# Performance work log

Measured on AMD Instinct MI355X. Metric: run time of the kernel, lower is better.

The kernel has to match this reference:

```python
import jax, jax.numpy as jnp
import numpy as np

B, S, T, E, H = 64, 256, 128, 256, 512


def setup_inputs() -> dict:
    key = jax.random.key(0)
    ks = jax.random.split(key, 12)
    sc = 0.05
    return {
        "trg_embed": jax.random.normal(ks[0], (B, T + 1, E), jnp.float32),
        "encoder_hidden": jax.random.normal(ks[1], (B, S, 2 * H), jnp.float32),
        "encoder_final": jax.random.normal(ks[2], (B, H), jnp.float32),
        "src_mask": jnp.ones((B, S), bool),
        "W_ih": jax.random.normal(ks[3], (3 * H, E + 2 * H), jnp.float32) * sc,
        "W_hh": jax.random.normal(ks[4], (3 * H, H), jnp.float32) * sc,
        "b_ih": jnp.zeros((3 * H,), jnp.float32),
        "b_hh": jnp.zeros((3 * H,), jnp.float32),
        "bridge_w": jax.random.normal(ks[5], (H, H), jnp.float32) * sc,
        "bridge_b": jnp.zeros((H,), jnp.float32),
        "key_w": jax.random.normal(ks[6], (H, 2 * H), jnp.float32) * sc,
        "query_w": jax.random.normal(ks[7], (H, H), jnp.float32) * sc,
        "energy_w": jax.random.normal(ks[8], (H,), jnp.float32) * sc,
        "pre_w": jax.random.normal(ks[9], (2 * H, H + 2 * H + E), jnp.float32) * sc,
        "pre_b": jnp.zeros((2 * H,), jnp.float32),
        "max_len": T,
    }


def reference(trg_embed, encoder_hidden, encoder_final, src_mask,
              W_ih, W_hh, b_ih, b_hh, bridge_w, bridge_b,
              key_w, query_w, energy_w, pre_w, pre_b, max_len):
    # bridge: initial decoder state from final encoder state
    h0 = jnp.tanh(encoder_final @ bridge_w.T + bridge_b)          # [B,H]
    # precomputed attention keys
    proj_key = jnp.einsum('bsk,hk->bsh', encoder_hidden, key_w)   # [B,S,H]
    neg = jnp.asarray(-1e9, trg_embed.dtype)

    prev = jnp.swapaxes(trg_embed[:, :max_len], 0, 1)             # [T,B,E]
    curr = jnp.swapaxes(trg_embed[:, 1:max_len + 1], 0, 1)        # [T,B,E] (generate_first)

    def step(h, pc):
        p, c = pc
        # --- additive (Bahdanau) attention, query = current hidden ---
        q = h @ query_w.T                                         # [B,H]
        scores = jnp.tanh(q[:, None, :] + proj_key) @ energy_w    # [B,S]
        scores = jnp.where(src_mask, scores, neg)
        alphas = jax.nn.softmax(scores, axis=-1)                  # [B,S]
        context = jnp.einsum('bs,bsd->bd', alphas, encoder_hidden)  # [B,2H]
        # --- generate_first: pre_output from previous hidden ---
        pre_out = jnp.concatenate([p, h, context], axis=-1) @ pre_w.T + pre_b  # [B,2H]
        # --- GRU cell (torch gate order r, z, n) ---
        x = jnp.concatenate([c, context], axis=-1)                # [B,E+2H]
        gi = x @ W_ih.T + b_ih
        gh = h @ W_hh.T + b_hh
        ir, iz, inn = jnp.split(gi, 3, axis=-1)
        hr, hz, hn = jnp.split(gh, 3, axis=-1)
        r = jax.nn.sigmoid(ir + hr)
        z = jax.nn.sigmoid(iz + hz)
        n = jnp.tanh(inn + r * hn)
        h_new = (1 - z) * n + z * h
        return h_new, (h_new, pre_out, alphas)

    h_fin, (states, pre_outs, attns) = jax.lax.scan(step, h0, (prev, curr))
    return (jnp.swapaxes(states, 0, 1),      # [B,T,H] decoder_states
            h_fin,                            # [B,H] final hidden
            jnp.swapaxes(pre_outs, 0, 1),     # [B,T,2H] pre_output_vectors
            jnp.swapaxes(attns, 0, 1))        # [B,T,S] attention_vectors
```

## Files before the change

kernel.cpp:

```cpp
#include <hip/hip_runtime.h>
#include <hip/hip_fp16.h>

using u32 = unsigned int;

constexpr int B = 64, S = 256, T = 128, E = 256, H = 512, H2 = 1024;
constexpr int TE = (T + 1) * E;

constexpr size_t OUT_HFIN = (size_t)B * T * H;
constexpr size_t OUT_PRE  = OUT_HFIN + (size_t)B * H;
constexpr size_t OUT_ATT  = OUT_PRE + (size_t)B * T * H2;

constexpr size_t WS_HPREV = 0;
constexpr size_t WS_QWT4  = 32768;
constexpr size_t WS_TRGT  = WS_QWT4 + 131072;
constexpr size_t WS_PK2   = WS_TRGT + 1056768;
constexpr size_t WS_HT2R  = WS_PK2 + 4194304;
constexpr size_t WS_QBUF  = WS_HT2R + 129 * 16384;
constexpr size_t WS_CTXR  = WS_QBUF + (size_t)128 * 16384;
constexpr size_t WS_SEWR  = WS_CTXR + (size_t)128 * 32768;
constexpr size_t WS_BAR   = WS_SEWR + 32768;
constexpr size_t WS_TOTAL = WS_BAR + 1024;

constexpr int L_EHS  = 0;
constexpr int L_EW   = 131072;
constexpr int L_HP   = 133376;
constexpr int L_SH2  = 134400;
constexpr int L_QRED = 135424;
constexpr int L_SHQ  = 135424;
constexpr int L_SCP  = 137728;
constexpr int L_SE   = 142080;
constexpr int L_CPAR = 142336;
constexpr int L_CRE1 = 135424;
constexpr int L_CRC  = 139520;
constexpr int L_SST  = 151808;
constexpr int SMEM_BYTES = 155904;

typedef _Float16 half8 __attribute__((ext_vector_type(8)));
typedef float    f32x4 __attribute__((ext_vector_type(4)));
union UH  { u32 u; _Float16 h[2]; };
union UH8 { uint4 v; half8 h; };

__device__ __forceinline__ u32 pkh(float a, float b) {
  auto v = __builtin_amdgcn_cvt_pkrtz(a, b);
  u32 r; __builtin_memcpy(&r, &v, 4); return r;
}
__device__ __forceinline__ float f16lo(u32 u) { UH x; x.u = u; return (float)x.h[0]; }
__device__ __forceinline__ float f16hi(u32 u) { UH x; x.u = u; return (float)x.h[1]; }

#if __has_builtin(__builtin_amdgcn_fdot2)
__device__ __forceinline__ float fdot2(u32 a, u32 b, float c) {
  typedef _Float16 h2t __attribute__((ext_vector_type(2)));
  h2t av, bv; __builtin_memcpy(&av, &a, 4); __builtin_memcpy(&bv, &b, 4);
  return __builtin_amdgcn_fdot2(av, bv, c, false);
}
#else
__device__ __forceinline__ float fdot2(u32 a, u32 b, float c) {
  return c + f16lo(a) * f16lo(b) + f16hi(a) * f16hi(b);
}
#endif

__device__ __forceinline__ float fast_tanh(float x) {
  return 1.0f - 2.0f / (__expf(2.0f * x) + 1.0f);
}
__device__ __forceinline__ float fast_sigmoid(float x) {
  return 1.0f / (1.0f + __expf(-x));
}
__device__ __forceinline__ float dot4(float4 a, float4 b) {
  return a.x * b.x + a.y * b.y + a.z * b.z + a.w * b.w;
}

__device__ __forceinline__ void st_wt(u32* p, u32 v) {
  __hip_atomic_store(p, v, __ATOMIC_RELAXED, __HIP_MEMORY_SCOPE_AGENT);
}
__device__ __forceinline__ void st_wt_f(float* p, float v) {
  union { float f; u32 u; } c; c.f = v;
  __hip_atomic_store((u32*)p, c.u, __ATOMIC_RELAXED, __HIP_MEMORY_SCOPE_AGENT);
}

__device__ __forceinline__ void gbar(u32* bar, int p, u32 n) {
  asm volatile("s_waitcnt vmcnt(0) lgkmcnt(0)" ::: "memory");
  __syncthreads();
  if (threadIdx.x == 0) {
    u32 old = __hip_atomic_fetch_add(bar + (p >> 4) * 32, 1u,
                                     __ATOMIC_RELAXED, __HIP_MEMORY_SCOPE_AGENT);
    if ((old & 15u) == 15u) {
      u32 r = __hip_atomic_fetch_add(bar + 768, 1u,
                                     __ATOMIC_RELAXED, __HIP_MEMORY_SCOPE_AGENT);
      if ((r & 15u) == 15u)
        __hip_atomic_store(bar + 800, n, __ATOMIC_RELAXED, __HIP_MEMORY_SCOPE_AGENT);
    }
    while (__hip_atomic_load(bar + 800, __ATOMIC_RELAXED,
                             __HIP_MEMORY_SCOPE_AGENT) < n)
      __builtin_amdgcn_s_sleep(2);
  }
  __syncthreads();
  asm volatile("" ::: "memory");
}

__global__ void bridge_kernel(const float* __restrict__ ef,
                              const float* __restrict__ bw,
                              const float* __restrict__ bb,
                              float* __restrict__ h0T) {
  int gid = blockIdx.x * blockDim.x + threadIdx.x;
  int j = gid >> 6, b = gid & 63;
  const float4* w = (const float4*)(bw + (size_t)j * H);
  const float4* e = (const float4*)(ef + (size_t)b * H);
  float acc = 0.f;
#pragma unroll 4
  for (int k = 0; k < H / 4; ++k) acc += dot4(w[k], e[k]);
  h0T[gid] = tanhf(acc + bb[j]);
}

__global__ void packh0_kernel(const float* __restrict__ hprevT, u32* __restrict__ hT2) {
  int idx = blockIdx.x * 512 + threadIdx.x;
  int dp = idx >> 6, b = idx & 63;
  hT2[(size_t)(dp >> 2) * 256 + b * 4 + (dp & 3)] =
      pkh(hprevT[(size_t)(2 * dp) * 64 + b], hprevT[(size_t)(2 * dp + 1) * 64 + b]);
}

__global__ void qwt4_kernel(const float* __restrict__ qw, uint4* __restrict__ qwt4) {
  int kq = blockIdx.x, j = threadIdx.x;
  const float* src = qw + (size_t)j * H + kq * 8;
  uint4 o;
  o.x = pkh(src[0], src[1]); o.y = pkh(src[2], src[3]);
  o.z = pkh(src[4], src[5]); o.w = pkh(src[6], src[7]);
  qwt4[(size_t)kq * 512 + j] = o;
}

__global__ void trgT2_kernel(const float* __restrict__ trg, u32* __restrict__ trgT) {
  int b = blockIdx.x, tid = threadIdx.x;
  for (int i = 0; i < 33; ++i) {
    int idx = i * 512 + tid;
    if (idx >= 129 * 128) break;
    int tt = idx >> 7, kp = idx & 127;
    float2 v = *(const float2*)(trg + (size_t)b * TE + (size_t)tt * 256 + kp * 2);
    trgT[(size_t)tt * 8192 + (size_t)(kp >> 2) * 256 + b * 4 + (kp & 3)] = pkh(v.x, v.y);
  }
}

__global__ void __launch_bounds__(256, 4) projkey2_kernel(
    const float* __restrict__ eh, const float* __restrict__ key_w,
    u32* __restrict__ pk) {
  constexpr int ST = 68;
  __shared__ float ea[64][ST];
  __shared__ float kb[64][ST];
  const int b  = blockIdx.x;
  const int s0 = blockIdx.y * 64;
  const int j0 = blockIdx.z * 64;
  const int tid = threadIdx.x;
  const int rl = tid >> 2, ql = tid & 3;
  const int tx = tid & 15, ty = tid >> 4;
  float acc[4][4] = {};
  const float* esrc = eh + ((size_t)b * S + s0 + rl) * H2;
  const float* ksrc = key_w + (size_t)(j0 + rl) * H2;
  for (int kc = 0; kc < H2; kc += 64) {
    float4 ev[4], kv[4];
#pragma unroll
    for (int m = 0; m < 4; ++m) {
      ev[m] = *(const float4*)(esrc + kc + ql * 16 + m * 4);
      kv[m] = *(const float4*)(ksrc + kc + ql * 16 + m * 4);
    }
    __syncthreads();
#pragma unroll
    for (int m = 0; m < 4; ++m) {
#pragma unroll
      for (int c = 0; c < 4; ++c) {
        int k = ql * 16 + m * 4 + c;
        ea[k][rl] = (&ev[m].x)[c];
        kb[k][rl] = (&kv[m].x)[c];
      }
    }
    __syncthreads();
#pragma unroll 8
    for (int k = 0; k < 64; ++k) {
      float4 a4 = *(const float4*)&ea[k][ty * 4];
      float4 b4 = *(const float4*)&kb[k][tx * 4];
      float av[4] = {a4.x, a4.y, a4.z, a4.w};
      float bv[4] = {b4.x, b4.y, b4.z, b4.w};
#pragma unroll
      for (int i = 0; i < 4; ++i)
#pragma unroll
        for (int jj = 0; jj < 4; ++jj) acc[i][jj] += av[i] * bv[jj];
    }
  }
#pragma unroll
  for (int i = 0; i < 4; ++i) {
    int s = s0 + ty * 4 + i;
    u32 u0 = pkh(acc[i][0], acc[i][1]);
    u32 u1 = pkh(acc[i][2], acc[i][3]);
    *(uint2*)(pk + (size_t)(b * S + s) * 256 + j0 / 2 + tx * 2) = make_uint2(u0, u1);
  }
}

#define MFMA_STEP(areg, bsrc, kq, acc) do {                                   \
    UH8 a_, b_;                                                               \
    a_.v = (areg);                                                            \
    b_.v = *(const uint4*)((bsrc) + (size_t)(((kq) * 4 + g4) * 256 + bcol * 4)); \
    (acc) = __builtin_amdgcn_mfma_f32_16x16x32_f16(a_.h, b_.h, (acc), 0, 0, 0); \
  } while (0)

__global__ void __launch_bounds__(1024) decoder_loop(
    const float* __restrict__ eh,
    const float* __restrict__ W_ih, const float* __restrict__ W_hh,
    const float* __restrict__ b_ih, const float* __restrict__ b_hh,
    const float* __restrict__ energy_w,
    const float* __restrict__ pre_w, const float* __restrict__ pre_b,
    float* __restrict__ out, float* __restrict__ ws) {
  __builtin_amdgcn_fence(__ATOMIC_ACQUIRE, "agent");

  extern __shared__ char smem[];
  u32*   ehs  = (u32*)(smem + L_EHS);
  float* ew2  = (float*)(smem + L_EW);
  float* shp  = (float*)(smem + L_HP);
  u32*   sh2  = (u32*)(smem + L_SH2);
  float* qred = (float*)(smem + L_QRED);
  float* shq  = (float*)(smem + L_SHQ);
  float* scp  = (float*)(smem + L_SCP);
  float* sse  = (float*)(smem + L_SE);
  float* cpar = (float*)(smem + L_CPAR);
  float* cre1 = (float*)(smem + L_CRE1);
  float* crc  = (float*)(smem + L_CRC);
  float* sst  = (float*)(smem + L_SST);

  const uint4* qwt4 = (const uint4*)(ws + WS_QWT4);
  const u32* trgT = (const u32*)(ws + WS_TRGT);
  const u32* pk2  = (const u32*)(ws + WS_PK2);
  u32*   ht2r = (u32*)(ws + WS_HT2R);
  u32*   qbr  = (u32*)(ws + WS_QBUF);
  u32*   ctxr = (u32*)(ws + WS_CTXR);
  float* sewr = ws + WS_SEWR;
  u32*   bar  = (u32*)(ws + WS_BAR);

  const int p = blockIdx.x, tid = threadIdx.x;
  const int lane = tid & 63, wid = tid >> 6;
  const int b = p >> 2, sib = p & 3, s0 = sib * 64;
  const int bt = wid & 3, kseg = wid >> 2;
  const int bcol = bt * 16 + (lane & 15);
  const int g4 = lane >> 4;

  for (int idx = tid; idx < 64 * 512; idx += 1024) {
    int s = idx >> 9, dp = idx & 511;
    float2 v = *(const float2*)(eh + (size_t)(b * 256 + s0 + s) * 1024 + 2 * dp);
    ehs[idx] = pkh(v.x, v.y);
  }
  if (tid < 512) ew2[(tid >> 5) * 36 + (tid & 31)] = energy_w[tid];
  uint4 regA[14];
  if (p < 192) {
    const bool isGate = p < 128;
#pragma unroll
    for (int k = 0; k < 14; ++k) {
      int ks = kseg * 14 + k;
      u32 w4[4];
#pragma unroll
      for (int i = 0; i < 4; ++i) {
        int kp = ks * 16 + (lane >> 4) * 4 + i;
        float a = 0.f, bv = 0.f;
        if (isGate) {
          int row = lane & 15, jo = row >> 2, g = row & 3;
          int j = p * 4 + jo;
          if (kp < 128) {
            if (g < 3) { const float* s_ = W_ih + (size_t)(g * 512 + j) * 1280 + kp * 2; a = s_[0]; bv = s_[1]; }
          } else if (kp < 384) {
            int c = (kp - 128) * 2;
            if (g < 2)       { const float* s_ = W_hh + (size_t)(g * 512 + j) * 512 + c; a = s_[0]; bv = s_[1]; }
            else if (g == 3) { const float* s_ = W_hh + (size_t)(1024 + j) * 512 + c;    a = s_[0]; bv = s_[1]; }
          } else {
            if (g < 3) { const float* s_ = W_ih + (size_t)(g * 512 + j) * 1280 + 256 + (kp - 384) * 2; a = s_[0]; bv = s_[1]; }
          }
        } else {
          int row = (p - 128) * 16 + (lane & 15);
          int c = (kp < 128) ? kp * 2 : (kp < 384) ? 256 + (kp - 128) * 2 : 768 + (kp - 384) * 2;
          const float* s_ = pre_w + (size_t)row * 1792 + c;
          a = s_[0]; bv = s_[1];
        }
        w4[i] = pkh(a, bv);
      }
      regA[k] = make_uint4(w4[0], w4[1], w4[2], w4[3]);
    }
    if (isGate && tid < 256) {
      int jo = tid >> 6, b2 = tid & 63;
      shp[tid] = ws[WS_HPREV + (size_t)(p * 4 + jo) * 64 + b2];
    }
  }
  __syncthreads();

  u32 bid = 0;
  for (int t = 0; t < T; ++t) {
    u32* ht2c = ht2r + (size_t)t * 16384;
    u32* ht2n = ht2r + (size_t)(t + 1) * 16384;
    u32* qbt  = qbr + (size_t)t * 16384;
    u32* ctxt = ctxr + (size_t)t * 32768;

    if (t > 0 && tid < 64) {
      float4 sv = *(const float4*)(sewr + (size_t)(t - 1) * 256 + (b << 2));
      float rinv = 1.f / (sv.x + sv.y + sv.z + sv.w);
      out[OUT_ATT + ((size_t)b * T + (t - 1)) * 256 + s0 + tid] *= rinv;
    }
    if (tid < 256)
      sh2[tid] = ht2c[(size_t)(tid >> 2) * 256 + b * 4 + (tid & 3)];
    __syncthreads();
    {
      const int jl = tid & 127, ks8 = tid >> 7;
      const int j = sib * 128 + jl;
      float acc = 0.f;
#pragma unroll
      for (int kk = 0; kk < 8; ++kk) {
        int kq = ks8 * 8 + kk;
        uint4 w = qwt4[(size_t)kq * 512 + j];
        acc = fdot2(w.x, sh2[kq * 4 + 0], acc);
        acc = fdot2(w.y, sh2[kq * 4 + 1], acc);
        acc = fdot2(w.z, sh2[kq * 4 + 2], acc);
        acc = fdot2(w.w, sh2[kq * 4 + 3], acc);
      }
      qred[jl * 8 + ks8] = acc;
    }
    __syncthreads();
    if (tid < 64) {
      float q0 = 0.f, q1 = 0.f;
#pragma unroll
      for (int i = 0; i < 8; ++i) { q0 += qred[(2 * tid) * 8 + i]; q1 += qred[(2 * tid + 1) * 8 + i]; }
      st_wt(qbt + (size_t)b * 256 + sib * 64 + tid, pkh(q0, q1));
    }
    gbar(bar, p, ++bid);

    if (tid < 256) {
      u32 qv = qbt[(size_t)b * 256 + tid];
      int j0 = 2 * tid;
      shq[(j0 >> 5) * 36 + (j0 & 31)] = f16lo(qv);
      shq[(j0 >> 5) * 36 + ((j0 & 31) + 1)] = f16hi(qv);
    }
    __syncthreads();
    {
      const int s = tid >> 4, jo = tid & 15;
      const uint4* pq = (const uint4*)(pk2 + (size_t)(b * 256 + s0 + s) * 256) + jo * 4;
      const float* q8 = shq + jo * 36;
      const float* e8 = ew2 + jo * 36;
      float acc = 0.f;
#pragma unroll
      for (int i = 0; i < 4; ++i) {
        uint4 v = pq[i];
        const float* qq = q8 + i * 8;
        const float* ee = e8 + i * 8;
#pragma unroll
        for (int c = 0; c < 4; ++c) {
          u32 w = (&v.x)[c];
          acc += fast_tanh(qq[2 * c] + f16lo(w)) * ee[2 * c] +
                 fast_tanh(qq[2 * c + 1] + f16hi(w)) * ee[2 * c + 1];
        }
      }
      scp[s * 17 + jo] = acc;
    }
    __syncthreads();
    if (tid < 64) {
      float sc = 0.f;
#pragma unroll
      for (int i = 0; i < 16; ++i) sc += scp[tid * 17 + i];
      float e = __expf(sc);
      out[OUT_ATT + ((size_t)b * T + t) * 256 + s0 + tid] = e;
      sse[tid] = e;
      float ssum = e;
      for (int d = 32; d; d >>= 1) ssum += __shfl_xor(ssum, d);
      if (tid == 0) st_wt_f(sewr + (size_t)t * 256 + p, ssum);
    }
    __syncthreads();
    {
      const int dp = tid & 511, sh = tid >> 9;
      float a0 = 0.f, a1 = 0.f;
      const u32* er = ehs + (sh * 32) * 512 + dp;
#pragma unroll 8
      for (int s = 0; s < 32; ++s) {
        u32 uu = er[s * 512];
        float es = sse[sh * 32 + s];
        a0 += es * f16lo(uu);
        a1 += es * f16hi(uu);
      }
      cpar[dp * 4 + sh * 2 + 0] = a0;
      cpar[dp * 4 + sh * 2 + 1] = a1;
    }
    __syncthreads();
    if (tid < 512) {
      float a0 = cpar[tid * 4 + 0] + cpar[tid * 4 + 2];
      float a1 = cpar[tid * 4 + 1] + cpar[tid * 4 + 3];
      __half2 v2 = __floats2half2_rn(a0, a1);
      unsafeAtomicAdd((__half2*)(ctxt + (size_t)(tid >> 2) * 256 + b * 4 + (tid & 3)), v2);
    }
    gbar(bar, p, ++bid);

    if (p < 192) {
      const bool isGate = p < 128;
      const u32* embB = trgT + (size_t)(isGate ? t + 1 : t) * 8192;
      f32x4 ceh = {0.f, 0.f, 0.f, 0.f}, cct = {0.f, 0.f, 0.f, 0.f};
      if (kseg == 0) {
#pragma unroll
        for (int k = 0; k < 8; ++k) MFMA_STEP(regA[k], embB, k, ceh);
#pragma unroll
        for (int k = 0; k < 6; ++k) MFMA_STEP(regA[8 + k], ht2c, k, ceh);
      } else if (kseg == 1) {
#pragma unroll
        for (int k = 0; k < 10; ++k) MFMA_STEP(regA[k], ht2c, 6 + k, ceh);
#pragma unroll
        for (int k = 0; k < 4; ++k) MFMA_STEP(regA[10 + k], ctxt, k, cct);
      } else if (kseg == 2) {
#pragma unroll
        for (int k = 0; k < 14; ++k) MFMA_STEP(regA[k], ctxt, 4 + k, cct);
      } else {
#pragma unroll
        for (int k = 0; k < 14; ++k) MFMA_STEP(regA[k], ctxt, 18 + k, cct);
      }
      if (kseg != 0) {
        float* cc = crc + (size_t)((kseg - 1) * 256 + bt * 64 + lane) * 4;
        cc[0] = cct[0]; cc[1] = cct[1]; cc[2] = cct[2]; cc[3] = cct[3];
        if (kseg == 1) {
          float* ce = cre1 + (size_t)(bt * 64 + lane) * 4;
          ce[0] = ceh[0]; ce[1] = ceh[1]; ce[2] = ceh[2]; ce[3] = ceh[3];
        }
      }
      __syncthreads();
      if (kseg == 0) {
        const float* ce = cre1 + (size_t)(bt * 64 + lane) * 4;
        const float* c0 = crc + (size_t)(0 * 256 + bt * 64 + lane) * 4;
        const float* c1 = crc + (size_t)(1 * 256 + bt * 64 + lane) * 4;
        const float* c2 = crc + (size_t)(2 * 256 + bt * 64 + lane) * 4;
        float4 sv = *(const float4*)(sewr + (size_t)t * 256 + (bcol << 2));
        float rv = 1.f / (sv.x + sv.y + sv.z + sv.w);
        float eh0 = ceh[0] + ce[0], eh1 = ceh[1] + ce[1];
        float eh2_ = ceh[2] + ce[2], eh3 = ceh[3] + ce[3];
        float ct0 = (c0[0] + c1[0] + c2[0]) * rv;
        float ct1 = (c0[1] + c1[1] + c2[1]) * rv;
        float ct2 = (c0[2] + c1[2] + c2[2]) * rv;
        float ct3 = (c0[3] + c1[3] + c2[3]) * rv;
        if (isGate) {
          int j = p * 4 + g4;
          float r = fast_sigmoid(eh0 + ct0 + b_ih[j] + b_hh[j]);
          float z = fast_sigmoid(eh1 + ct1 + b_ih[512 + j] + b_hh[512 + j]);
          float n = fast_tanh((eh2_ + ct2 + b_ih[1024 + j]) +
                              r * (eh3 + b_hh[1024 + j]));
          float hp = shp[g4 * 64 + bcol];
          float hv = (1.f - z) * n + z * hp;
          shp[g4 * 64 + bcol] = hv;
          float ho = __shfl_xor(hv, 16);
          if ((g4 & 1) == 0) {
            int jp = p * 2 + (g4 >> 1);
            st_wt(ht2n + (size_t)(jp >> 2) * 256 + bcol * 4 + (jp & 3), pkh(hv, ho));
          }
          sst[g4 * 64 + bcol] = hv;
        } else {
          int prow = (p - 128) * 16 + g4 * 4;
          sst[(g4 * 4 + 0) * 64 + bcol] = eh0 + ct0 + pre_b[prow + 0];
          sst[(g4 * 4 + 1) * 64 + bcol] = eh1 + ct1 + pre_b[prow + 1];
          sst[(g4 * 4 + 2) * 64 + bcol] = eh2_ + ct2 + pre_b[prow + 2];
          sst[(g4 * 4 + 3) * 64 + bcol] = eh3 + ct3 + pre_b[prow + 3];
        }
      }
      __syncthreads();
      if (isGate) {
        if (tid < 64) {
          int b2 = tid;
          float4 o = make_float4(sst[0 * 64 + b2], sst[1 * 64 + b2],
                                 sst[2 * 64 + b2], sst[3 * 64 + b2]);
          *(float4*)(out + ((size_t)b2 * T + t) * 512 + p * 4) = o;
          if (t == T - 1)
            *(float4*)(out + OUT_HFIN + (size_t)b2 * 512 + p * 4) = o;
        }
      } else {
        if (tid < 256) {
          int b2 = tid & 63, q4 = tid >> 6;
          float4 o = make_float4(sst[(q4 * 4 + 0) * 64 + b2], sst[(q4 * 4 + 1) * 64 + b2],
                                 sst[(q4 * 4 + 2) * 64 + b2], sst[(q4 * 4 + 3) * 64 + b2]);
          *(float4*)(out + OUT_PRE + ((size_t)b2 * T + t) * 1024 + (p - 128) * 16 + q4 * 4) = o;
        }
      }
    }
    gbar(bar, p, ++bid);
  }

  if (tid < 64) {
    float4 sv = *(const float4*)(sewr + (size_t)(T - 1) * 256 + (b << 2));
    float rinv = 1.f / (sv.x + sv.y + sv.z + sv.w);
    out[OUT_ATT + ((size_t)b * T + (T - 1)) * 256 + s0 + tid] *= rinv;
  }
}

extern "C" void kernel_launch(void* const* d_in, const int* in_sizes, int n_in,
                              void* d_out, int out_size, void* d_ws, size_t ws_size,
                              hipStream_t stream) {
  const float* trg      = (const float*)d_in[0];
  const float* eh       = (const float*)d_in[1];
  const float* ef       = (const float*)d_in[2];
  const float* W_ih     = (const float*)d_in[4];
  const float* W_hh     = (const float*)d_in[5];
  const float* b_ih     = (const float*)d_in[6];
  const float* b_hh     = (const float*)d_in[7];
  const float* bridge_w = (const float*)d_in[8];
  const float* bridge_b = (const float*)d_in[9];
  const float* key_w    = (const float*)d_in[10];
  const float* query_w  = (const float*)d_in[11];
  const float* energy_w = (const float*)d_in[12];
  const float* pre_w    = (const float*)d_in[13];
  const float* pre_b    = (const float*)d_in[14];
  float* out = (float*)d_out;
  float* ws  = (float*)d_ws;

  hipMemsetAsync((char*)d_ws + WS_CTXR * sizeof(float), 0,
                 (WS_TOTAL - WS_CTXR) * sizeof(float), stream);
  bridge_kernel<<<64, 512, 0, stream>>>(ef, bridge_w, bridge_b, ws + WS_HPREV);
  packh0_kernel<<<32, 512, 0, stream>>>(ws + WS_HPREV, (u32*)(ws + WS_HT2R));
  qwt4_kernel<<<64, 512, 0, stream>>>(query_w, (uint4*)(ws + WS_QWT4));
  trgT2_kernel<<<64, 512, 0, stream>>>(trg, (u32*)(ws + WS_TRGT));
  projkey2_kernel<<<dim3(B, S / 64, H / 64), 256, 0, stream>>>(eh, key_w,
                                                               (u32*)(ws + WS_PK2));

  hipFuncSetAttribute((const void*)decoder_loop,
                      hipFuncAttributeMaxDynamicSharedMemorySize, SMEM_BYTES);
  void* args[10];
  args[0] = (void*)&eh;
  args[1] = (void*)&W_ih;    args[2] = (void*)&W_hh;
  args[3] = (void*)&b_ih;    args[4] = (void*)&b_hh;
  args[5] = (void*)&energy_w;
  args[6] = (void*)&pre_w;   args[7] = (void*)&pre_b;
  args[8] = (void*)&out;     args[9] = (void*)&ws;
  hipLaunchCooperativeKernel((const void*)decoder_loop, dim3(256), dim3(1024),
                             args, SMEM_BYTES, stream);
}
```

Baseline: 3.773 ms.

## Stream pre-packed weight fragments from global; keep projected keys in registers

```diff
diff --git a/kernel.cpp b/kernel.cpp
--- a/kernel.cpp
+++ b/kernel.cpp
@@ -19,7 +19,8 @@
 constexpr size_t WS_CTXR  = WS_QBUF + (size_t)128 * 16384;
 constexpr size_t WS_SEWR  = WS_CTXR + (size_t)128 * 32768;
 constexpr size_t WS_BAR   = WS_SEWR + 32768;
-constexpr size_t WS_TOTAL = WS_BAR + 1024;
+constexpr size_t WS_WFR   = WS_BAR + 1024;
+constexpr size_t WS_TOTAL = WS_WFR + (size_t)192 * 3584 * 4;
 
 constexpr int L_EHS  = 0;
 constexpr int L_EW   = 131072;
@@ -135,6 +136,43 @@
     int tt = idx >> 7, kp = idx & 127;
     float2 v = *(const float2*)(trg + (size_t)b * TE + (size_t)tt * 256 + kp * 2);
     trgT[(size_t)tt * 8192 + (size_t)(kp >> 2) * 256 + b * 4 + (kp & 3)] = pkh(v.x, v.y);
+  }
+}
+
+__global__ void wfrag_kernel(const float* __restrict__ W_ih,
+                             const float* __restrict__ W_hh,
+                             const float* __restrict__ pre_w,
+                             uint4* __restrict__ wfr) {
+  const int p = blockIdx.x;
+  const bool isGate = p < 128;
+  for (int idx = threadIdx.x; idx < 56 * 64; idx += 512) {
+    int ks = idx >> 6, lane = idx & 63;
+    u32 w4[4];
+#pragma unroll
+    for (int i = 0; i < 4; ++i) {
+      int kp = ks * 16 + (lane >> 4) * 4 + i;
+      float a = 0.f, bv = 0.f;
+      if (isGate) {
+        int row = lane & 15, jo = row >> 2, g = row & 3;
+        int j = p * 4 + jo;
+        if (kp < 128) {
+          if (g < 3) { const float* s_ = W_ih + (size_t)(g * 512 + j) * 1280 + kp * 2; a = s_[0]; bv = s_[1]; }
+        } else if (kp < 384) {
+          int c = (kp - 128) * 2;
+          if (g < 2)       { const float* s_ = W_hh + (size_t)(g * 512 + j) * 512 + c; a = s_[0]; bv = s_[1]; }
+          else if (g == 3) { const float* s_ = W_hh + (size_t)(1024 + j) * 512 + c;    a = s_[0]; bv = s_[1]; }
+        } else {
+          if (g < 3) { const float* s_ = W_ih + (size_t)(g * 512 + j) * 1280 + 256 + (kp - 384) * 2; a = s_[0]; bv = s_[1]; }
+        }
+      } else {
+        int row = (p - 128) * 16 + (lane & 15);
+        int c = (kp < 128) ? kp * 2 : (kp < 384) ? 256 + (kp - 128) * 2 : 768 + (kp - 384) * 2;
+        const float* s_ = pre_w + (size_t)row * 1792 + c;
+        a = s_[0]; bv = s_[1];
+      }
+      w4[i] = pkh(a, bv);
+    }
+    wfr[(size_t)p * 3584 + idx] = make_uint4(w4[0], w4[1], w4[2], w4[3]);
   }
 }
 
@@ -192,19 +230,17 @@
   }
 }
 
-#define MFMA_STEP(areg, bsrc, kq, acc) do {                                   \
+#define MFMA_STEP(k, bsrc, kq, acc) do {                                      \
     UH8 a_, b_;                                                               \
-    a_.v = (areg);                                                            \
+    a_.v = wfp[(size_t)(k) * 64];                                             \
     b_.v = *(const uint4*)((bsrc) + (size_t)(((kq) * 4 + g4) * 256 + bcol * 4)); \
     (acc) = __builtin_amdgcn_mfma_f32_16x16x32_f16(a_.h, b_.h, (acc), 0, 0, 0); \
   } while (0)
 
 __global__ void __launch_bounds__(1024) decoder_loop(
     const float* __restrict__ eh,
-    const float* __restrict__ W_ih, const float* __restrict__ W_hh,
     const float* __restrict__ b_ih, const float* __restrict__ b_hh,
-    const float* __restrict__ energy_w,
-    const float* __restrict__ pre_w, const float* __restrict__ pre_b,
+    const float* __restrict__ energy_w, const float* __restrict__ pre_b,
     float* __restrict__ out, float* __restrict__ ws) {
   __builtin_amdgcn_fence(__ATOMIC_ACQUIRE, "agent");
 
@@ -225,6 +261,7 @@
   const uint4* qwt4 = (const uint4*)(ws + WS_QWT4);
   const u32* trgT = (const u32*)(ws + WS_TRGT);
   const u32* pk2  = (const u32*)(ws + WS_PK2);
+  const uint4* wfru = (const uint4*)(ws + WS_WFR);
   u32*   ht2r = (u32*)(ws + WS_HT2R);
   u32*   qbr  = (u32*)(ws + WS_QBUF);
   u32*   ctxr = (u32*)(ws + WS_CTXR);
@@ -244,43 +281,17 @@
     ehs[idx] = pkh(v.x, v.y);
   }
   if (tid < 512) ew2[(tid >> 5) * 36 + (tid & 31)] = energy_w[tid];
-  uint4 regA[14];
-  if (p < 192) {
-    const bool isGate = p < 128;
-#pragma unroll
-    for (int k = 0; k < 14; ++k) {
-      int ks = kseg * 14 + k;
-      u32 w4[4];
-#pragma unroll
-      for (int i = 0; i < 4; ++i) {
-        int kp = ks * 16 + (lane >> 4) * 4 + i;
-        float a = 0.f, bv = 0.f;
-        if (isGate) {
-          int row = lane & 15, jo = row >> 2, g = row & 3;
-          int j = p * 4 + jo;
-          if (kp < 128) {
-            if (g < 3) { const float* s_ = W_ih + (size_t)(g * 512 + j) * 1280 + kp * 2; a = s_[0]; bv = s_[1]; }
-          } else if (kp < 384) {
-            int c = (kp - 128) * 2;
-            if (g < 2)       { const float* s_ = W_hh + (size_t)(g * 512 + j) * 512 + c; a = s_[0]; bv = s_[1]; }
-            else if (g == 3) { const float* s_ = W_hh + (size_t)(1024 + j) * 512 + c;    a = s_[0]; bv = s_[1]; }
-          } else {
-            if (g < 3) { const float* s_ = W_ih + (size_t)(g * 512 + j) * 1280 + 256 + (kp - 384) * 2; a = s_[0]; bv = s_[1]; }
-          }
-        } else {
-          int row = (p - 128) * 16 + (lane & 15);
-          int c = (kp < 128) ? kp * 2 : (kp < 384) ? 256 + (kp - 128) * 2 : 768 + (kp - 384) * 2;
-          const float* s_ = pre_w + (size_t)row * 1792 + c;
-          a = s_[0]; bv = s_[1];
-        }
-        w4[i] = pkh(a, bv);
-      }
-      regA[k] = make_uint4(w4[0], w4[1], w4[2], w4[3]);
-    }
-    if (isGate && tid < 256) {
-      int jo = tid >> 6, b2 = tid & 63;
-      shp[tid] = ws[WS_HPREV + (size_t)(p * 4 + jo) * 64 + b2];
-    }
+  if (p < 128 && tid < 256) {
+    int jo = tid >> 6, b2 = tid & 63;
+    shp[tid] = ws[WS_HPREV + (size_t)(p * 4 + jo) * 64 + b2];
+  }
+  u32 pkr[16];
+  {
+    const u32* pq = pk2 + (size_t)(b * 256 + s0 + (tid >> 4)) * 256 + (tid & 15) * 16;
+#pragma unroll
+    for (int i = 0; i < 16; ++i) pkr[i] = pq[i];
+#pragma unroll
+    for (int i = 0; i < 16; ++i) asm volatile("" : "+v"(pkr[i]));
   }
   __syncthreads();
 
@@ -332,18 +343,16 @@
     __syncthreads();
     {
       const int s = tid >> 4, jo = tid & 15;
-      const uint4* pq = (const uint4*)(pk2 + (size_t)(b * 256 + s0 + s) * 256) + jo * 4;
       const float* q8 = shq + jo * 36;
       const float* e8 = ew2 + jo * 36;
       float acc = 0.f;
 #pragma unroll
       for (int i = 0; i < 4; ++i) {
-        uint4 v = pq[i];
         const float* qq = q8 + i * 8;
         const float* ee = e8 + i * 8;
 #pragma unroll
         for (int c = 0; c < 4; ++c) {
-          u32 w = (&v.x)[c];
+          u32 w = pkr[i * 4 + c];
           acc += fast_tanh(qq[2 * c] + f16lo(w)) * ee[2 * c] +
                  fast_tanh(qq[2 * c + 1] + f16hi(w)) * ee[2 * c + 1];
         }
@@ -389,23 +398,24 @@
     if (p < 192) {
       const bool isGate = p < 128;
       const u32* embB = trgT + (size_t)(isGate ? t + 1 : t) * 8192;
+      const uint4* wfp = wfru + ((size_t)p * 56 + (size_t)kseg * 14) * 64 + lane;
       f32x4 ceh = {0.f, 0.f, 0.f, 0.f}, cct = {0.f, 0.f, 0.f, 0.f};
       if (kseg == 0) {
 #pragma unroll
-        for (int k = 0; k < 8; ++k) MFMA_STEP(regA[k], embB, k, ceh);
-#pragma unroll
-        for (int k = 0; k < 6; ++k) MFMA_STEP(regA[8 + k], ht2c, k, ceh);
+        for (int k = 0; k < 8; ++k) MFMA_STEP(k, embB, k, ceh);
+#pragma unroll
+        for (int k = 0; k < 6; ++k) MFMA_STEP(8 + k, ht2c, k, ceh);
       } else if (kseg == 1) {
 #pragma unroll
-        for (int k = 0; k < 10; ++k) MFMA_STEP(regA[k], ht2c, 6 + k, ceh);
-#pragma unroll
-        for (int k = 0; k < 4; ++k) MFMA_STEP(regA[10 + k], ctxt, k, cct);
+        for (int k = 0; k < 10; ++k) MFMA_STEP(k, ht2c, 6 + k, ceh);
+#pragma unroll
+        for (int k = 0; k < 4; ++k) MFMA_STEP(10 + k, ctxt, k, cct);
       } else if (kseg == 2) {
 #pragma unroll
-        for (int k = 0; k < 14; ++k) MFMA_STEP(regA[k], ctxt, 4 + k, cct);
+        for (int k = 0; k < 14; ++k) MFMA_STEP(k, ctxt, 4 + k, cct);
       } else {
 #pragma unroll
-        for (int k = 0; k < 14; ++k) MFMA_STEP(regA[k], ctxt, 18 + k, cct);
+        for (int k = 0; k < 14; ++k) MFMA_STEP(k, ctxt, 18 + k, cct);
       }
       if (kseg != 0) {
         float* cc = crc + (size_t)((kseg - 1) * 256 + bt * 64 + lane) * 4;
@@ -502,23 +512,22 @@
   float* ws  = (float*)d_ws;
 
   hipMemsetAsync((char*)d_ws + WS_CTXR * sizeof(float), 0,
-                 (WS_TOTAL - WS_CTXR) * sizeof(float), stream);
+                 (WS_WFR - WS_CTXR) * sizeof(float), stream);
   bridge_kernel<<<64, 512, 0, stream>>>(ef, bridge_w, bridge_b, ws + WS_HPREV);
   packh0_kernel<<<32, 512, 0, stream>>>(ws + WS_HPREV, (u32*)(ws + WS_HT2R));
   qwt4_kernel<<<64, 512, 0, stream>>>(query_w, (uint4*)(ws + WS_QWT4));
   trgT2_kernel<<<64, 512, 0, stream>>>(trg, (u32*)(ws + WS_TRGT));
+  wfrag_kernel<<<192, 512, 0, stream>>>(W_ih, W_hh, pre_w, (uint4*)(ws + WS_WFR));
   projkey2_kernel<<<dim3(B, S / 64, H / 64), 256, 0, stream>>>(eh, key_w,
                                                                (u32*)(ws + WS_PK2));
 
   hipFuncSetAttribute((const void*)decoder_loop,
                       hipFuncAttributeMaxDynamicSharedMemorySize, SMEM_BYTES);
-  void* args[10];
+  void* args[7];
   args[0] = (void*)&eh;
-  args[1] = (void*)&W_ih;    args[2] = (void*)&W_hh;
-  args[3] = (void*)&b_ih;    args[4] = (void*)&b_hh;
-  args[5] = (void*)&energy_w;
-  args[6] = (void*)&pre_w;   args[7] = (void*)&pre_b;
-  args[8] = (void*)&out;     args[9] = (void*)&ws;
+  args[1] = (void*)&b_ih;    args[2] = (void*)&b_hh;
+  args[3] = (void*)&energy_w; args[4] = (void*)&pre_b;
+  args[5] = (void*)&out;     args[6] = (void*)&ws;
   hipLaunchCooperativeKernel((const void*)decoder_loop, dim3(256), dim3(1024),
                              args, SMEM_BYTES, stream);
 }
```

Measured after the change: 3.932 ms. 4.2% more time.
